# Performance work log

Hardware: AMD Instinct MI355X
Metric: run time of the kernel (lower is better)

## Reference

```python
import jax, jax.numpy as jnp
import numpy as np

D = 192          # embed_dim
DI = 2 * D       # d_inner (Mamba expand=2)
R = 12           # dt_rank = ceil(D / d_state)
N = 16           # d_state
DEPTH = 24
P = 16           # patch size
B = 4
SS, TS = 256, 128
PT = (TS // P) ** 2   # 64 template patches
PS = (SS // P) ** 2   # 256 search patches
L = PT + PS + 1       # 321 tokens (middle cls)


def setup_inputs() -> dict:
    key = jax.random.key(0)
    ks = jax.random.split(key, 24)
    f = lambda k, shp, s=0.02: (jax.random.normal(k, shp) * s).astype(jnp.float32)
    Alog = jnp.log(jnp.arange(1, N + 1, dtype=jnp.float32))  # S4D-real init
    Alog = jnp.tile(Alog, (DEPTH, DI, 1))
    return {
        "x_search": f(ks[0], (B, 3, SS, SS), 1.0),
        "x_template": f(ks[1], (B, 3, TS, TS), 1.0),
        "patch_w": f(ks[2], (D, 3, P, P)),
        "patch_b": jnp.zeros((D,), jnp.float32),
        "cls_token": f(ks[3], (1, 1, D)),
        "pos_embed": f(ks[4], (1, L, D)),
        "Win": f(ks[5], (DEPTH, 2 * DI, D)),
        "convw": f(ks[6], (DEPTH, DI, 4), 0.2),
        "convb": jnp.zeros((DEPTH, DI), jnp.float32),
        "Wx": f(ks[7], (DEPTH, R + 2 * N, DI)),
        "Wdt": f(ks[8], (DEPTH, DI, R), 0.1),
        "bdt": f(ks[9], (DEPTH, DI), 0.1),
        "Alog": Alog,
        "Dp": jnp.ones((DEPTH, DI), jnp.float32),
        "convw_b": f(ks[10], (DEPTH, DI, 4), 0.2),
        "convb_b": jnp.zeros((DEPTH, DI), jnp.float32),
        "Wx_b": f(ks[11], (DEPTH, R + 2 * N, DI)),
        "Wdt_b": f(ks[12], (DEPTH, DI, R), 0.1),
        "bdt_b": f(ks[13], (DEPTH, DI), 0.1),
        "Alog_b": Alog,
        "Dp_b": jnp.ones((DEPTH, DI), jnp.float32),
        "Wout": f(ks[14], (DEPTH, D, DI)),
        "normw": jnp.ones((DEPTH, D), jnp.float32),
        "normw_f": jnp.ones((D,), jnp.float32),
    }


def silu(x):
    return x * jax.nn.sigmoid(x)


def rmsnorm(x, w, eps=1e-5):
    return x * jax.lax.rsqrt(jnp.mean(x * x, -1, keepdims=True) + eps) * w


def patch_embed(x, w, b):
    # non-overlapping patch conv == blocked reshape + einsum
    Bn, C, H, W = x.shape
    xp = x.reshape(Bn, C, H // P, P, W // P, P)
    t = jnp.einsum('bcipjq,dcpq->bijd', xp, w)
    return t.reshape(Bn, (H // P) * (W // P), -1) + b


def causal_conv(u, w, b):
    # depthwise causal conv, kernel 4: u [B,DI,L], w [DI,4]
    Lx = u.shape[-1]
    up = jnp.pad(u, ((0, 0), (0, 0), (3, 0)))
    y = sum(w[:, k][None, :, None] * up[:, :, k:k + Lx] for k in range(4))
    return y + b[None, :, None]


def selective_scan(u, delta, A, Bm, Cm, Dp):
    # u, delta: [B,DI,L]; A: [DI,N]; Bm, Cm: [B,N,L]
    dA = jnp.exp(jnp.einsum('bdl,dn->lbdn', delta, A))
    dBu = jnp.einsum('bdl,bnl->lbdn', delta * u, Bm)

    def step(h, inp):
        dAt, dBut, ct = inp
        h = dAt * h + dBut
        return h, jnp.einsum('bdn,bn->bd', h, ct)

    h0 = jnp.zeros((u.shape[0], DI, N), u.dtype)
    _, ys = jax.lax.scan(step, h0, (dA, dBu, Cm.transpose(2, 0, 1)))
    y = ys.transpose(1, 2, 0)  # [B,DI,L]
    return y + Dp[None, :, None] * u


def _branch(x, z, convw, convb, Wx, Wdt, bdt, Alog, Dp):
    xc = silu(causal_conv(x, convw, convb))
    xdbl = jnp.einsum('bdl,ed->ble', xc, Wx)
    dt, Bm, Cm = xdbl[..., :R], xdbl[..., R:R + N], xdbl[..., R + N:]
    delta = jax.nn.softplus(jnp.einsum('blr,dr->bdl', dt, Wdt) + bdt[None, :, None])
    y = selective_scan(xc, delta, -jnp.exp(Alog), Bm.transpose(0, 2, 1),
                       Cm.transpose(0, 2, 1), Dp)
    return y * silu(z)


def _mixer(h, p):
    xz = jnp.einsum('bld,ed->ble', h, p['Win'])
    x = xz[..., :DI].transpose(0, 2, 1)   # [B,DI,L]
    z = xz[..., DI:].transpose(0, 2, 1)
    y = _branch(x, z, p['convw'], p['convb'], p['Wx'], p['Wdt'], p['bdt'],
                p['Alog'], p['Dp'])
    yb = _branch(x[..., ::-1], z[..., ::-1], p['convw_b'], p['convb_b'], p['Wx_b'],
                 p['Wdt_b'], p['bdt_b'], p['Alog_b'], p['Dp_b'])
    out = (y + yb[..., ::-1]) * 0.5  # bimamba v2 with if_divide_out
    return jnp.einsum('bdl,od->blo', out, p['Wout'])


def reference(x_search, x_template, patch_w, patch_b, cls_token, pos_embed,
              Win, convw, convb, Wx, Wdt, bdt, Alog, Dp,
              convw_b, convb_b, Wx_b, Wdt_b, bdt_b, Alog_b, Dp_b,
              Wout, normw, normw_f):
    ts = patch_embed(x_template, patch_w, patch_b)   # [B,64,D]
    ss = patch_embed(x_search, patch_w, patch_b)     # [B,256,D]
    tok = jnp.concatenate([ts, ss], 1)               # [B,320,D]
    mid = tok.shape[1] // 2
    cls = jnp.broadcast_to(cls_token, (tok.shape[0], 1, D))
    tok = jnp.concatenate([tok[:, :mid], cls, tok[:, mid:]], 1) + pos_embed

    lp = {'Win': Win, 'convw': convw, 'convb': convb, 'Wx': Wx, 'Wdt': Wdt,
          'bdt': bdt, 'Alog': Alog, 'Dp': Dp, 'convw_b': convw_b,
          'convb_b': convb_b, 'Wx_b': Wx_b, 'Wdt_b': Wdt_b, 'bdt_b': bdt_b,
          'Alog_b': Alog_b, 'Dp_b': Dp_b, 'Wout': Wout, 'normw': normw}

    def layer_step(carry, p):
        hidden, residual = carry
        residual = hidden + residual           # add
        hn = rmsnorm(residual, p['normw'])     # norm (fused_add_norm semantics)
        hidden = _mixer(hn, p)                 # mamba mixer
        return (hidden, residual), None

    (hidden, residual), _ = jax.lax.scan(layer_step, (tok, jnp.zeros_like(tok)), lp)
    return rmsnorm(hidden + residual, normw_f)   # final add + norm, [B,321,D]
```

## Files before the change

kernel.cpp:

```cpp
#include <hip/hip_runtime.h>
#include <math.h>

#define B_ 4
#define L_ 321
#define D_ 192
#define DI_ 384
#define E_ 768
#define R_ 12
#define N_ 16
#define DEPTH_ 24
#define XD 44

#define NC_ 21
#define LC_ 16

typedef __attribute__((ext_vector_type(8))) short bf16x8;
typedef __attribute__((ext_vector_type(4))) float f32x4;
typedef unsigned short ushort_t;

__device__ __forceinline__ float silu_f(float x) { return x / (1.f + __expf(-x)); }

__device__ __forceinline__ ushort_t f2bf(float x) {
    union { float f; unsigned u; } v; v.f = x;
    return (ushort_t)((v.u + 0x7fffu + ((v.u >> 16) & 1u)) >> 16);
}
__device__ __forceinline__ float bf2f(ushort_t h) {
    union { unsigned u; float f; } v; v.u = ((unsigned)h) << 16; return v.f;
}

__global__ void cvt_bf16(const float* __restrict__ src, ushort_t* __restrict__ dst, int n) {
    for (int i = blockIdx.x * blockDim.x + threadIdx.x; i < n; i += gridDim.x * blockDim.x)
        dst[i] = f2bf(src[i]);
}

__global__ void im2col_kernel(const float* __restrict__ xs, const float* __restrict__ xt,
                              ushort_t* __restrict__ pm) {
    int p_all = blockIdx.x % 320;
    int b = blockIdx.x / 320;
    const float* src; int i, j, W;
    if (p_all < 64) { int p = p_all; i = p >> 3; j = p & 7; W = 128; src = xt + (size_t)b*3*128*128; }
    else            { int p = p_all - 64; i = p >> 4; j = p & 15; W = 256; src = xs + (size_t)b*3*256*256; }
    ushort_t* dst = pm + (size_t)blockIdx.x * 768;
    for (int m = threadIdx.x; m < 768; m += blockDim.x) {
        int c = m >> 8, rem = m & 255, pp = rem >> 4, qq = rem & 15;
        dst[m] = f2bf(src[(size_t)(c*W + i*16 + pp)*W + j*16 + qq]);
    }
}

__global__ void tok_scatter(const float* __restrict__ tokmat, const float* __restrict__ pb,
                            const float* __restrict__ cls, const float* __restrict__ pos,
                            float* __restrict__ hidden, float* __restrict__ residual) {
    int blk = blockIdx.x;
    int b = blk / L_, t = blk % L_;
    int d = threadIdx.x;
    size_t o = (size_t)(b*L_ + t)*D_ + d;
    residual[o] = 0.f;
    float v;
    if (t == 160) v = cls[d];
    else {
        int p = (t < 160) ? t : t - 1;
        v = tokmat[(size_t)(b*320 + p)*D_ + d] + pb[d];
    }
    hidden[o] = v + pos[t*D_ + d];
}

template<int WM, int WN, int MFR, int NFR, int AMODE>
__device__ __forceinline__ void mfma_gemm_body(const ushort_t* __restrict__ A,
                                               const float* __restrict__ Af0,
                                               const float* __restrict__ Af1,
                                               const ushort_t* __restrict__ Bw,
                                               float* __restrict__ C,
                                               int M, int N, int K, int bx, int by) {
    constexpr int BM = WM * MFR * 16;
    constexpr int BN = WN * NFR * 16;
    int wave = threadIdx.x >> 6, lane = threadIdx.x & 63;
    int wr = wave / WN, wc = wave % WN;
    int m0 = by * BM + wr * MFR * 16;
    int n0 = bx * BN + wc * NFR * 16;
    int lrow = lane & 15;
    int lk   = (lane >> 4) * 8;

    f32x4 acc[MFR][NFR];
#pragma unroll
    for (int i = 0; i < MFR; ++i)
#pragma unroll
        for (int j = 0; j < NFR; ++j) acc[i][j] = (f32x4){0.f, 0.f, 0.f, 0.f};

    for (int k0 = 0; k0 < K; k0 += 32) {
        bf16x8 a[MFR], b[NFR];
#pragma unroll
        for (int i = 0; i < MFR; ++i) {
            int r = m0 + i*16 + lrow; r = min(r, M - 1);
            if (AMODE == 0) {
                a[i] = *(const bf16x8*)(A + (size_t)r*K + k0 + lk);
            } else {
                const float* p0 = Af0 + (size_t)r*K + k0 + lk;
                const float* p1 = Af1 + (size_t)r*K + k0 + lk;
                bf16x8 t;
#pragma unroll
                for (int j = 0; j < 8; ++j) t[j] = (short)f2bf(0.5f*(p0[j] + p1[j]));
                a[i] = t;
            }
        }
#pragma unroll
        for (int jn = 0; jn < NFR; ++jn) {
            int c = n0 + jn*16 + lrow; c = min(c, N - 1);
            b[jn] = *(const bf16x8*)(Bw + (size_t)c*K + k0 + lk);
        }
#pragma unroll
        for (int i = 0; i < MFR; ++i)
#pragma unroll
            for (int jn = 0; jn < NFR; ++jn)
                acc[i][jn] = __builtin_amdgcn_mfma_f32_16x16x32_bf16(a[i], b[jn], acc[i][jn], 0, 0, 0);
    }

    int crow = (lane >> 4) * 4;
    int ccol = lane & 15;
#pragma unroll
    for (int i = 0; i < MFR; ++i)
#pragma unroll
        for (int jn = 0; jn < NFR; ++jn) {
            int c = n0 + jn*16 + ccol;
            if (c >= N) continue;
#pragma unroll
            for (int j = 0; j < 4; ++j) {
                int r = m0 + i*16 + crow + j;
                if (r < M) C[(size_t)r*N + c] = acc[i][jn][j];
            }
        }
}

template<int WM, int WN, int MFR, int NFR, int AMODE>
__global__ __launch_bounds__(WM*WN*64) void mfma_gemm(const ushort_t* __restrict__ A,
                          const float* __restrict__ Af0, const float* __restrict__ Af1,
                          const ushort_t* __restrict__ Bw, float* __restrict__ C,
                          int M, int N, int K) {
    mfma_gemm_body<WM, WN, MFR, NFR, AMODE>(A, Af0, Af1, Bw, C, M, N, K, blockIdx.x, blockIdx.y);
}

__global__ __launch_bounds__(256) void mfma_gemm_dual(const ushort_t* __restrict__ A0, const ushort_t* __restrict__ B0, float* __restrict__ C0,
                               const ushort_t* __restrict__ A1, const ushort_t* __restrict__ B1, float* __restrict__ C1,
                               int M, int N, int K) {
    if (blockIdx.z)
        mfma_gemm_body<4, 1, 1, 3, 0>(A1, nullptr, nullptr, B1, C1, M, N, K, blockIdx.x, blockIdx.y);
    else
        mfma_gemm_body<4, 1, 1, 3, 0>(A0, nullptr, nullptr, B0, C0, M, N, K, blockIdx.x, blockIdx.y);
}

__global__ void prenorm_kernel(float* __restrict__ residual, const float* __restrict__ hidden,
                               const float* __restrict__ normw, ushort_t* __restrict__ hn) {
    int row = blockIdx.x;
    int tid = threadIdx.x;
    __shared__ float red[256];
    float v = 0.f;
    if (tid < D_) {
        v = residual[(size_t)row*D_ + tid] + hidden[(size_t)row*D_ + tid];
        residual[(size_t)row*D_ + tid] = v;
    }
    red[tid] = v * v;
    __syncthreads();
    for (int s = 128; s > 0; s >>= 1) { if (tid < s) red[tid] += red[tid + s]; __syncthreads(); }
    float scale = rsqrtf(red[0] / (float)D_ + 1e-5f);
    if (tid < D_) hn[(size_t)row*D_ + tid] = f2bf(v * scale * normw[tid]);
}

__global__ void final_kernel(const float* __restrict__ residual, const float* __restrict__ hidden,
                             const float* __restrict__ normw_f, float* __restrict__ out) {
    int row = blockIdx.x;
    int tid = threadIdx.x;
    __shared__ float red[256];
    float v = 0.f;
    if (tid < D_) v = residual[(size_t)row*D_ + tid] + hidden[(size_t)row*D_ + tid];
    red[tid] = v * v;
    __syncthreads();
    for (int s = 128; s > 0; s >>= 1) { if (tid < s) red[tid] += red[tid + s]; __syncthreads(); }
    float scale = rsqrtf(red[0] / (float)D_ + 1e-5f);
    if (tid < D_) out[(size_t)row*D_ + tid] = v * scale * normw_f[tid];
}

__global__ void conv_kernel(const ushort_t* __restrict__ xz,
                            const float* __restrict__ cw, const float* __restrict__ cb,
                            const float* __restrict__ cwb, const float* __restrict__ cbb,
                            ushort_t* __restrict__ xc_f, ushort_t* __restrict__ xc_b) {
    int blk = blockIdx.x;
    int b = blk / L_, l = blk % L_;
    int d = threadIdx.x;
    const ushort_t* xbase = xz + (size_t)b*L_*E_ + d;
    float acc = cb[d];
#pragma unroll
    for (int k = 0; k < 4; ++k) {
        int t = l - 3 + k;
        if (t >= 0) acc = fmaf(cw[d*4 + k], bf2f(xbase[(size_t)t*E_]), acc);
    }
    xc_f[(size_t)(b*L_ + l)*DI_ + d] = f2bf(silu_f(acc));
    float accb = cbb[d];
#pragma unroll
    for (int k = 0; k < 4; ++k) {
        int t = l - 3 + k;
        if (t >= 0) accb = fmaf(cwb[d*4 + k], bf2f(xbase[(size_t)(L_ - 1 - t)*E_]), accb);
    }
    xc_b[(size_t)(b*L_ + l)*DI_ + d] = f2bf(silu_f(accb));
}

__global__ void scan_part1(const ushort_t* __restrict__ xc_f, const ushort_t* __restrict__ xc_b,
                           const float* __restrict__ xdbl_f, const float* __restrict__ xdbl_b,
                           const float* __restrict__ Wdt, const float* __restrict__ bdt,
                           const float* __restrict__ Wdtb, const float* __restrict__ bdtb,
                           const float* __restrict__ Alog, const float* __restrict__ Alogb,
                           float* __restrict__ hloc, float* __restrict__ aprod) {
    int c = blockIdx.x, b = blockIdx.y, br = blockIdx.z;
    int d = threadIdx.x;
    const ushort_t* xc = br ? xc_b : xc_f;
    const float* xd = br ? xdbl_b : xdbl_f;
    const float* Wd = br ? Wdtb : Wdt;
    const float* bd = br ? bdtb : bdt;
    const float* Al = br ? Alogb : Alog;
    __shared__ float su[LC_][DI_];
    __shared__ float sdt[LC_][R_];
    __shared__ float sB[LC_][N_];
    int lbeg = c * LC_;
    int lend = min(lbeg + LC_, L_);
    int len = lend - lbeg;
    for (int l2 = 0; l2 < len; ++l2) {
        size_t row = (size_t)b*L_ + lbeg + l2;
        su[l2][d] = bf2f(xc[row*DI_ + d]);
    }
    for (int idx = d; idx < len*N_; idx += DI_) {
        int l2 = idx >> 4, n = idx & 15;
        sB[l2][n] = xd[((size_t)b*L_ + lbeg + l2)*XD + R_ + n];
    }
    for (int idx = d; idx < len*R_; idx += DI_) {
        int l2 = idx / R_, r = idx % R_;
        sdt[l2][r] = xd[((size_t)b*L_ + lbeg + l2)*XD + r];
    }
    __syncthreads();
    float wreg[R_];
#pragma unroll
    for (int r = 0; r < R_; ++r) wreg[r] = Wd[d*R_ + r];
    float bdv = bd[d];
    float a[N_];
#pragma unroll
    for (int n = 0; n < N_; ++n) a[n] = -__expf(Al[d*N_ + n]);
    float h[N_], ap[N_];
#pragma unroll
    for (int n = 0; n < N_; ++n) { h[n] = 0.f; ap[n] = 1.f; }
    for (int l2 = 0; l2 < len; ++l2) {
        float dacc = bdv;
#pragma unroll
        for (int r = 0; r < R_; ++r) dacc = fmaf(wreg[r], sdt[l2][r], dacc);
        float dv = fmaxf(dacc, 0.f) + log1pf(__expf(-fabsf(dacc)));
        float u = su[l2][d], du = dv * u;
#pragma unroll
        for (int n = 0; n < N_; ++n) {
            float e = __expf(dv * a[n]);
            h[n] = fmaf(e, h[n], du * sB[l2][n]);
            ap[n] *= e;
        }
    }
    size_t base = (((size_t)(b*2 + br)*NC_ + c)*N_)*DI_ + d;
#pragma unroll
    for (int n = 0; n < N_; ++n) {
        hloc[base + (size_t)n*DI_]  = h[n];
        aprod[base + (size_t)n*DI_] = ap[n];
    }
}

__global__ void scan_combine(const float* __restrict__ hloc, const float* __restrict__ aprod,
                             float* __restrict__ hin) {
    int g = blockIdx.x * blockDim.x + threadIdx.x;
    int bb = g / (N_ * DI_);
    int rem = g % (N_ * DI_);
    float hrun = 0.f;
    for (int c = 0; c < NC_; ++c) {
        size_t idx = ((size_t)bb*NC_ + c)*N_*DI_ + rem;
        hin[idx] = hrun;
        hrun = fmaf(aprod[idx], hrun, hloc[idx]);
    }
}

__global__ void scan_part3(const ushort_t* __restrict__ xc_f, const ushort_t* __restrict__ xc_b,
                           const float* __restrict__ xdbl_f, const float* __restrict__ xdbl_b,
                           const float* __restrict__ Wdt, const float* __restrict__ bdt,
                           const float* __restrict__ Wdtb, const float* __restrict__ bdtb,
                           const ushort_t* __restrict__ xz,
                           const float* __restrict__ Alog, const float* __restrict__ Alogb,
                           const float* __restrict__ Dpf, const float* __restrict__ Dpb,
                           const float* __restrict__ hin,
                           float* __restrict__ y_f, float* __restrict__ y_b) {
    int c = blockIdx.x, b = blockIdx.y, br = blockIdx.z;
    int d = threadIdx.x;
    const ushort_t* xc = br ? xc_b : xc_f;
    const float* xd = br ? xdbl_b : xdbl_f;
    const float* Wd = br ? Wdtb : Wdt;
    const float* bd = br ? bdtb : bdt;
    const float* Al = br ? Alogb : Alog;
    const float* Dpp = br ? Dpb : Dpf;
    float* y = br ? y_b : y_f;
    __shared__ float su[LC_][DI_];
    __shared__ float sdt[LC_][R_];
    __shared__ float sB[LC_][N_];
    __shared__ float sC[LC_][N_];
    int lbeg = c * LC_;
    int lend = min(lbeg + LC_, L_);
    int len = lend - lbeg;
    for (int l2 = 0; l2 < len; ++l2) {
        size_t row = (size_t)b*L_ + lbeg + l2;
        su[l2][d] = bf2f(xc[row*DI_ + d]);
    }
    for (int idx = d; idx < len*N_; idx += DI_) {
        int l2 = idx >> 4, n = idx & 15;
        size_t row = (size_t)b*L_ + lbeg + l2;
        sB[l2][n] = xd[row*XD + R_ + n];
        sC[l2][n] = xd[row*XD + R_ + N_ + n];
    }
    for (int idx = d; idx < len*R_; idx += DI_) {
        int l2 = idx / R_, r = idx % R_;
        sdt[l2][r] = xd[((size_t)b*L_ + lbeg + l2)*XD + r];
    }
    __syncthreads();
    float wreg[R_];
#pragma unroll
    for (int r = 0; r < R_; ++r) wreg[r] = Wd[d*R_ + r];
    float bdv = bd[d];
    float a[N_];
#pragma unroll
    for (int n = 0; n < N_; ++n) a[n] = -__expf(Al[d*N_ + n]);
    float h[N_];
    size_t hbase = (((size_t)(b*2 + br)*NC_ + c)*N_)*DI_ + d;
#pragma unroll
    for (int n = 0; n < N_; ++n) h[n] = hin[hbase + (size_t)n*DI_];
    float dpv = Dpp[d];
    for (int l2 = 0; l2 < len; ++l2) {
        float dacc = bdv;
#pragma unroll
        for (int r = 0; r < R_; ++r) dacc = fmaf(wreg[r], sdt[l2][r], dacc);
        float dv = fmaxf(dacc, 0.f) + log1pf(__expf(-fabsf(dacc)));
        float u = su[l2][d], du = dv * u;
        float yv = 0.f;
#pragma unroll
        for (int n = 0; n < N_; ++n) {
            float e = __expf(dv * a[n]);
            h[n] = fmaf(e, h[n], du * sB[l2][n]);
            yv = fmaf(h[n], sC[l2][n], yv);
        }
        yv = fmaf(dpv, u, yv);
        int lo = br ? (L_ - 1 - (lbeg + l2)) : (lbeg + l2);
        float zv = bf2f(xz[((size_t)b*L_ + lo)*E_ + DI_ + d]);
        y[((size_t)b*L_ + lo)*DI_ + d] = yv * silu_f(zv);
    }
}

extern "C" void kernel_launch(void* const* d_in, const int* in_sizes, int n_in,
                              void* d_out, int out_size, void* d_ws, size_t ws_size,
                              hipStream_t stream) {
    const float* xs     = (const float*)d_in[0];
    const float* xt     = (const float*)d_in[1];
    const float* pw     = (const float*)d_in[2];
    const float* pb     = (const float*)d_in[3];
    const float* cls    = (const float*)d_in[4];
    const float* pos    = (const float*)d_in[5];
    const float* Win    = (const float*)d_in[6];
    const float* convw  = (const float*)d_in[7];
    const float* convb  = (const float*)d_in[8];
    const float* Wx     = (const float*)d_in[9];
    const float* Wdt    = (const float*)d_in[10];
    const float* bdt    = (const float*)d_in[11];
    const float* Alog   = (const float*)d_in[12];
    const float* Dp     = (const float*)d_in[13];
    const float* convwb = (const float*)d_in[14];
    const float* convbb = (const float*)d_in[15];
    const float* Wxb    = (const float*)d_in[16];
    const float* Wdtb   = (const float*)d_in[17];
    const float* bdtb   = (const float*)d_in[18];
    const float* Alogb  = (const float*)d_in[19];
    const float* Dpb    = (const float*)d_in[20];
    const float* Wout   = (const float*)d_in[21];
    const float* normw  = (const float*)d_in[22];
    const float* normwf = (const float*)d_in[23];
    float* out = (float*)d_out;

    float* ws = (float*)d_ws;
    size_t off = 0;
    auto alloc = [&](size_t nfloats) { float* p = ws + off; off += nfloats; return p; };
    const size_t BL = (size_t)B_ * L_;
    const size_t CHNK = (size_t)B_ * 2 * NC_ * N_ * DI_;

    float*    residual = alloc(BL * D_);
    float*    hidden   = alloc(BL * D_);
    ushort_t* hn_bf    = (ushort_t*)alloc(BL * D_ / 2);
    ushort_t* xzb_bf   = (ushort_t*)alloc(BL * E_ / 2);
    ushort_t* xcf_bf   = (ushort_t*)alloc(BL * DI_ / 2);
    ushort_t* xcb_bf   = (ushort_t*)alloc(BL * DI_ / 2);
    float*    xdbl_f   = alloc(BL * XD);
    float*    xdbl_b   = alloc(BL * XD);
    float*    y_f      = alloc(BL * DI_);
    float*    y_b      = alloc(BL * DI_);
    float*    hloc     = alloc(CHNK);
    float*    aprod    = alloc(CHNK);
    float*    hin      = alloc(CHNK);
    ushort_t* pw_bf    = (ushort_t*)alloc((size_t)D_ * 768 / 2);
    ushort_t* Win_bf   = (ushort_t*)alloc((size_t)DEPTH_ * E_ * D_ / 2);
    ushort_t* Wx_bf    = (ushort_t*)alloc((size_t)DEPTH_ * XD * DI_ / 2);
    ushort_t* Wxb_bf   = (ushort_t*)alloc((size_t)DEPTH_ * XD * DI_ / 2);
    ushort_t* Wout_bf  = (ushort_t*)alloc((size_t)DEPTH_ * D_ * DI_ / 2);
    (void)ws_size; (void)in_sizes; (void)n_in; (void)out_size;

    cvt_bf16<<<dim3(64),  dim3(256), 0, stream>>>(pw,   pw_bf,   D_ * 768);
    cvt_bf16<<<dim3(2048), dim3(256), 0, stream>>>(Win,  Win_bf,  DEPTH_ * E_ * D_);
    cvt_bf16<<<dim3(512), dim3(256), 0, stream>>>(Wx,   Wx_bf,   DEPTH_ * XD * DI_);
    cvt_bf16<<<dim3(512), dim3(256), 0, stream>>>(Wxb,  Wxb_bf,  DEPTH_ * XD * DI_);
    cvt_bf16<<<dim3(1024), dim3(256), 0, stream>>>(Wout, Wout_bf, DEPTH_ * D_ * DI_);

    ushort_t* pmat   = (ushort_t*)y_f;
    float*    tokmat = y_b;
    im2col_kernel<<<dim3(B_ * 320), dim3(256), 0, stream>>>(xs, xt, pmat);
    mfma_gemm<2, 2, 2, 2, 0><<<dim3(3, 20), dim3(256), 0, stream>>>(
        pmat, nullptr, nullptr, pw_bf, tokmat, B_ * 320, D_, 768);
    tok_scatter<<<dim3(B_ * L_), dim3(192), 0, stream>>>(tokmat, pb, cls, pos, hidden, residual);

    for (int layer = 0; layer < DEPTH_; ++layer) {
        const ushort_t* Win_l  = Win_bf  + (size_t)layer * E_ * D_;
        const ushort_t* Wx_l   = Wx_bf   + (size_t)layer * XD * DI_;
        const ushort_t* Wxb_l  = Wxb_bf  + (size_t)layer * XD * DI_;
        const ushort_t* Wout_l = Wout_bf + (size_t)layer * D_ * DI_;
        const float* cw_l    = convw  + (size_t)layer * DI_ * 4;
        const float* cb_l    = convb  + (size_t)layer * DI_;
        const float* cwb_l   = convwb + (size_t)layer * DI_ * 4;
        const float* cbb_l   = convbb + (size_t)layer * DI_;
        const float* Wdt_l   = Wdt    + (size_t)layer * DI_ * R_;
        const float* Wdtb_l  = Wdtb   + (size_t)layer * DI_ * R_;
        const float* bdt_l   = bdt    + (size_t)layer * DI_;
        const float* bdtb_l  = bdtb   + (size_t)layer * DI_;
        const float* Alog_l  = Alog   + (size_t)layer * DI_ * N_;
        const float* Alogb_l = Alogb  + (size_t)layer * DI_ * N_;
        const float* Dp_l    = Dp     + (size_t)layer * DI_;
        const float* Dpb_l   = Dpb    + (size_t)layer * DI_;
        const float* normw_l = normw  + (size_t)layer * D_;

        prenorm_kernel<<<dim3((int)BL), dim3(256), 0, stream>>>(residual, hidden, normw_l, hn_bf);
        mfma_gemm<2, 2, 2, 2, 0><<<dim3(12, 21), dim3(256), 0, stream>>>(
            hn_bf, nullptr, nullptr, Win_l, hloc , (int)BL, E_, D_);
        cvt_bf16<<<dim3(1024), dim3(256), 0, stream>>>(hloc, xzb_bf, (int)(BL * E_));
        conv_kernel<<<dim3((int)BL), dim3(DI_), 0, stream>>>(xzb_bf, cw_l, cb_l, cwb_l, cbb_l, xcf_bf, xcb_bf);
        mfma_gemm_dual<<<dim3(1, 21, 2), dim3(256), 0, stream>>>(
            xcf_bf, Wx_l, xdbl_f, xcb_bf, Wxb_l, xdbl_b, (int)BL, XD, DI_);
        scan_part1<<<dim3(NC_, B_, 2), dim3(DI_), 0, stream>>>(
            xcf_bf, xcb_bf, xdbl_f, xdbl_b, Wdt_l, bdt_l, Wdtb_l, bdtb_l,
            Alog_l, Alogb_l, hloc, aprod);
        scan_combine<<<dim3((B_*2*N_*DI_)/256), dim3(256), 0, stream>>>(hloc, aprod, hin);
        scan_part3<<<dim3(NC_, B_, 2), dim3(DI_), 0, stream>>>(
            xcf_bf, xcb_bf, xdbl_f, xdbl_b, Wdt_l, bdt_l, Wdtb_l, bdtb_l, xzb_bf,
            Alog_l, Alogb_l, Dp_l, Dpb_l, hin, y_f, y_b);
        mfma_gemm<2, 2, 2, 2, 1><<<dim3(3, 21), dim3(256), 0, stream>>>(
            nullptr, y_f, y_b, Wout_l, hidden, (int)BL, D_, DI_);
    }

    final_kernel<<<dim3((int)BL), dim3(256), 0, stream>>>(residual, hidden, normwf, out);
}
```

Before: 2.152 ms.

## Fuse conv into x-proj GEMM, out-proj with add+norm, bf16 in-proj output

The in-projection GEMM now writes bf16 directly, which drops the separate fp32-to-bf16 conversion pass. The causal depthwise conv plus SiLU is computed inside the x-projection MFMA kernel. The output projection is fused with the residual add and RMSNorm of the next layer, or the final norm on the last layer, which removes the per-layer prenorm and final kernels. Scan inner loops get a partial unroll for full-length chunks. Together these cut launches and memory round trips, at the cost of redundant conv reads per row tile and lower occupancy in the fused out-proj with only 41 blocks.

```diff
diff --git a/kernel.cpp b/kernel.cpp
--- a/kernel.cpp
+++ b/kernel.cpp
@@ -64,15 +64,14 @@
     hidden[o] = v + pos[t*D_ + d];
 }
 
-template<int WM, int WN, int MFR, int NFR, int AMODE>
-__device__ __forceinline__ void mfma_gemm_body(const ushort_t* __restrict__ A,
-                                               const float* __restrict__ Af0,
-                                               const float* __restrict__ Af1,
-                                               const ushort_t* __restrict__ Bw,
-                                               float* __restrict__ C,
-                                               int M, int N, int K, int bx, int by) {
+template<int WM, int WN, int MFR, int NFR, int CMODE>
+__global__ __launch_bounds__(WM*WN*64) void mfma_gemm(const ushort_t* __restrict__ A,
+                          const ushort_t* __restrict__ Bw,
+                          float* __restrict__ Cf, ushort_t* __restrict__ Ch,
+                          int M, int N, int K) {
     constexpr int BM = WM * MFR * 16;
     constexpr int BN = WN * NFR * 16;
+    int bx = blockIdx.x, by = blockIdx.y;
     int wave = threadIdx.x >> 6, lane = threadIdx.x & 63;
     int wr = wave / WN, wc = wave % WN;
     int m0 = by * BM + wr * MFR * 16;
@@ -91,16 +90,7 @@
 #pragma unroll
         for (int i = 0; i < MFR; ++i) {
             int r = m0 + i*16 + lrow; r = min(r, M - 1);
-            if (AMODE == 0) {
-                a[i] = *(const bf16x8*)(A + (size_t)r*K + k0 + lk);
-            } else {
-                const float* p0 = Af0 + (size_t)r*K + k0 + lk;
-                const float* p1 = Af1 + (size_t)r*K + k0 + lk;
-                bf16x8 t;
-#pragma unroll
-                for (int j = 0; j < 8; ++j) t[j] = (short)f2bf(0.5f*(p0[j] + p1[j]));
-                a[i] = t;
-            }
+            a[i] = *(const bf16x8*)(A + (size_t)r*K + k0 + lk);
         }
 #pragma unroll
         for (int jn = 0; jn < NFR; ++jn) {
@@ -125,26 +115,175 @@
 #pragma unroll
             for (int j = 0; j < 4; ++j) {
                 int r = m0 + i*16 + crow + j;
-                if (r < M) C[(size_t)r*N + c] = acc[i][jn][j];
+                if (r < M) {
+                    if (CMODE == 0) Cf[(size_t)r*N + c] = acc[i][jn][j];
+                    else            Ch[(size_t)r*N + c] = f2bf(acc[i][jn][j]);
+                }
             }
         }
 }
 
-template<int WM, int WN, int MFR, int NFR, int AMODE>
-__global__ __launch_bounds__(WM*WN*64) void mfma_gemm(const ushort_t* __restrict__ A,
-                          const float* __restrict__ Af0, const float* __restrict__ Af1,
-                          const ushort_t* __restrict__ Bw, float* __restrict__ C,
-                          int M, int N, int K) {
-    mfma_gemm_body<WM, WN, MFR, NFR, AMODE>(A, Af0, Af1, Bw, C, M, N, K, blockIdx.x, blockIdx.y);
-}
-
-__global__ __launch_bounds__(256) void mfma_gemm_dual(const ushort_t* __restrict__ A0, const ushort_t* __restrict__ B0, float* __restrict__ C0,
-                               const ushort_t* __restrict__ A1, const ushort_t* __restrict__ B1, float* __restrict__ C1,
-                               int M, int N, int K) {
-    if (blockIdx.z)
-        mfma_gemm_body<4, 1, 1, 3, 0>(A1, nullptr, nullptr, B1, C1, M, N, K, blockIdx.x, blockIdx.y);
-    else
-        mfma_gemm_body<4, 1, 1, 3, 0>(A0, nullptr, nullptr, B0, C0, M, N, K, blockIdx.x, blockIdx.y);
+__global__ __launch_bounds__(256) void conv_xdbl_dual(
+    const ushort_t* __restrict__ xz,
+    const float* __restrict__ cw, const float* __restrict__ cb,
+    const float* __restrict__ cwb, const float* __restrict__ cbb,
+    const ushort_t* __restrict__ Wxf, const ushort_t* __restrict__ Wxbw,
+    ushort_t* __restrict__ xc_f, ushort_t* __restrict__ xc_b,
+    float* __restrict__ xdbl_f, float* __restrict__ xdbl_b) {
+    constexpr int NFR = 3;
+    const int M = B_ * L_, Nn = XD, K = DI_;
+    int rev = blockIdx.z;
+    const float* cwp = rev ? cwb : cw;
+    const float* cbp = rev ? cbb : cb;
+    const ushort_t* Bw = rev ? Wxbw : Wxf;
+    ushort_t* xc = rev ? xc_b : xc_f;
+    float* Cout = rev ? xdbl_b : xdbl_f;
+
+    int wave = threadIdx.x >> 6, lane = threadIdx.x & 63;
+    int m0 = blockIdx.y * 64 + wave * 16;
+    int lrow = lane & 15;
+    int lk = (lane >> 4) * 8;
+
+    f32x4 acc[NFR];
+#pragma unroll
+    for (int jn = 0; jn < NFR; ++jn) acc[jn] = (f32x4){0.f, 0.f, 0.f, 0.f};
+
+    int rc = min(m0 + lrow, M - 1);
+    int b = rc / L_, l = rc % L_;
+    const ushort_t* xzb = xz + (size_t)b*L_*E_;
+
+    for (int k0 = 0; k0 < K; k0 += 32) {
+        int d0 = k0 + lk;
+        float xr[4][8];
+#pragma unroll
+        for (int k = 0; k < 4; ++k) {
+            int t = l - 3 + k;
+            if (t >= 0) {
+                int tr = rev ? (L_ - 1 - t) : t;
+                bf16x8 xv = *(const bf16x8*)(xzb + (size_t)tr*E_ + d0);
+#pragma unroll
+                for (int j = 0; j < 8; ++j) xr[k][j] = bf2f((ushort_t)xv[j]);
+            } else {
+#pragma unroll
+                for (int j = 0; j < 8; ++j) xr[k][j] = 0.f;
+            }
+        }
+        bf16x8 afrag;
+#pragma unroll
+        for (int j = 0; j < 8; ++j) {
+            float4 w4 = *(const float4*)(cwp + (size_t)(d0 + j) * 4);
+            float acv = cbp[d0 + j];
+            acv = fmaf(w4.x, xr[0][j], acv);
+            acv = fmaf(w4.y, xr[1][j], acv);
+            acv = fmaf(w4.z, xr[2][j], acv);
+            acv = fmaf(w4.w, xr[3][j], acv);
+            afrag[j] = (short)f2bf(silu_f(acv));
+        }
+        *(bf16x8*)(xc + (size_t)rc*DI_ + d0) = afrag;
+        bf16x8 bfr[NFR];
+#pragma unroll
+        for (int jn = 0; jn < NFR; ++jn) {
+            int c = min(jn*16 + lrow, Nn - 1);
+            bfr[jn] = *(const bf16x8*)(Bw + (size_t)c*K + k0 + lk);
+        }
+#pragma unroll
+        for (int jn = 0; jn < NFR; ++jn)
+            acc[jn] = __builtin_amdgcn_mfma_f32_16x16x32_bf16(afrag, bfr[jn], acc[jn], 0, 0, 0);
+    }
+    int crow = (lane >> 4) * 4, ccol = lane & 15;
+#pragma unroll
+    for (int jn = 0; jn < NFR; ++jn) {
+        int c = jn*16 + ccol;
+        if (c >= Nn) continue;
+#pragma unroll
+        for (int j = 0; j < 4; ++j) {
+            int rr = m0 + crow + j;
+            if (rr < M) Cout[(size_t)rr*Nn + c] = acc[jn][j];
+        }
+    }
+}
+
+template<bool LAST>
+__global__ __launch_bounds__(512) void outproj_fused(
+    const float* __restrict__ yf, const float* __restrict__ yb,
+    const ushort_t* __restrict__ Ww,
+    float* __restrict__ residual, const float* __restrict__ nw,
+    ushort_t* __restrict__ hn, float* __restrict__ outp) {
+    const int M = B_*L_, Nn = D_, K = DI_;
+    int wave = threadIdx.x >> 6, lane = threadIdx.x & 63;
+    int wr = wave >> 2, wc = wave & 3;
+    int m0 = blockIdx.x * 32 + wr * 16;
+    int n0 = wc * 48;
+    int lrow = lane & 15, lk = (lane >> 4) * 8;
+
+    f32x4 acc[3];
+#pragma unroll
+    for (int jn = 0; jn < 3; ++jn) acc[jn] = (f32x4){0.f, 0.f, 0.f, 0.f};
+
+    for (int k0 = 0; k0 < K; k0 += 32) {
+        int r = min(m0 + lrow, M - 1);
+        const float* p0 = yf + (size_t)r*K + k0 + lk;
+        const float* p1 = yb + (size_t)r*K + k0 + lk;
+        bf16x8 a;
+#pragma unroll
+        for (int j = 0; j < 8; ++j) a[j] = (short)f2bf(0.5f*(p0[j] + p1[j]));
+        bf16x8 bfr[3];
+#pragma unroll
+        for (int jn = 0; jn < 3; ++jn) {
+            int c = n0 + jn*16 + lrow;
+            bfr[jn] = *(const bf16x8*)(Ww + (size_t)c*K + k0 + lk);
+        }
+#pragma unroll
+        for (int jn = 0; jn < 3; ++jn)
+            acc[jn] = __builtin_amdgcn_mfma_f32_16x16x32_bf16(a, bfr[jn], acc[jn], 0, 0, 0);
+    }
+
+    int crow = (lane >> 4) * 4, ccol = lane & 15;
+    float resv[4][3];
+    float sq[4] = {0.f, 0.f, 0.f, 0.f};
+#pragma unroll
+    for (int j = 0; j < 4; ++j) {
+        int r = m0 + crow + j;
+        bool ok = r < M;
+#pragma unroll
+        for (int jn = 0; jn < 3; ++jn) {
+            int c = n0 + jn*16 + ccol;
+            float v = ok ? (residual[(size_t)r*Nn + c] + acc[jn][j]) : 0.f;
+            resv[j][jn] = v;
+            sq[j] = fmaf(v, v, sq[j]);
+        }
+    }
+#pragma unroll
+    for (int m = 1; m < 16; m <<= 1)
+#pragma unroll
+        for (int j = 0; j < 4; ++j) sq[j] += __shfl_xor(sq[j], m, 64);
+
+    __shared__ float part[32][4];
+    if (ccol == 0) {
+        int rt0 = wr*16 + crow;
+#pragma unroll
+        for (int j = 0; j < 4; ++j) part[rt0 + j][wc] = sq[j];
+    }
+    __syncthreads();
+#pragma unroll
+    for (int j = 0; j < 4; ++j) {
+        int r = m0 + crow + j;
+        if (r >= M) continue;
+        int rt = wr*16 + crow + j;
+        float tot = part[rt][0] + part[rt][1] + part[rt][2] + part[rt][3];
+        float scale = rsqrtf(tot / (float)Nn + 1e-5f);
+#pragma unroll
+        for (int jn = 0; jn < 3; ++jn) {
+            int c = n0 + jn*16 + ccol;
+            float v = resv[j][jn];
+            if (LAST) {
+                outp[(size_t)r*Nn + c] = v * scale * nw[c];
+            } else {
+                residual[(size_t)r*Nn + c] = v;
+                hn[(size_t)r*Nn + c] = f2bf(v * scale * nw[c]);
+            }
+        }
+    }
 }
 
 __global__ void prenorm_kernel(float* __restrict__ residual, const float* __restrict__ hidden,
@@ -162,44 +301,6 @@
     for (int s = 128; s > 0; s >>= 1) { if (tid < s) red[tid] += red[tid + s]; __syncthreads(); }
     float scale = rsqrtf(red[0] / (float)D_ + 1e-5f);
     if (tid < D_) hn[(size_t)row*D_ + tid] = f2bf(v * scale * normw[tid]);
-}
-
-__global__ void final_kernel(const float* __restrict__ residual, const float* __restrict__ hidden,
-                             const float* __restrict__ normw_f, float* __restrict__ out) {
-    int row = blockIdx.x;
-    int tid = threadIdx.x;
-    __shared__ float red[256];
-    float v = 0.f;
-    if (tid < D_) v = residual[(size_t)row*D_ + tid] + hidden[(size_t)row*D_ + tid];
-    red[tid] = v * v;
-    __syncthreads();
-    for (int s = 128; s > 0; s >>= 1) { if (tid < s) red[tid] += red[tid + s]; __syncthreads(); }
-    float scale = rsqrtf(red[0] / (float)D_ + 1e-5f);
-    if (tid < D_) out[(size_t)row*D_ + tid] = v * scale * normw_f[tid];
-}
-
-__global__ void conv_kernel(const ushort_t* __restrict__ xz,
-                            const float* __restrict__ cw, const float* __restrict__ cb,
-                            const float* __restrict__ cwb, const float* __restrict__ cbb,
-                            ushort_t* __restrict__ xc_f, ushort_t* __restrict__ xc_b) {
-    int blk = blockIdx.x;
-    int b = blk / L_, l = blk % L_;
-    int d = threadIdx.x;
-    const ushort_t* xbase = xz + (size_t)b*L_*E_ + d;
-    float acc = cb[d];
-#pragma unroll
-    for (int k = 0; k < 4; ++k) {
-        int t = l - 3 + k;
-        if (t >= 0) acc = fmaf(cw[d*4 + k], bf2f(xbase[(size_t)t*E_]), acc);
-    }
-    xc_f[(size_t)(b*L_ + l)*DI_ + d] = f2bf(silu_f(acc));
-    float accb = cbb[d];
-#pragma unroll
-    for (int k = 0; k < 4; ++k) {
-        int t = l - 3 + k;
-        if (t >= 0) accb = fmaf(cwb[d*4 + k], bf2f(xbase[(size_t)(L_ - 1 - t)*E_]), accb);
-    }
-    xc_b[(size_t)(b*L_ + l)*DI_ + d] = f2bf(silu_f(accb));
 }
 
 __global__ void scan_part1(const ushort_t* __restrict__ xc_f, const ushort_t* __restrict__ xc_b,
@@ -244,7 +345,8 @@
     float h[N_], ap[N_];
 #pragma unroll
     for (int n = 0; n < N_; ++n) { h[n] = 0.f; ap[n] = 1.f; }
-    for (int l2 = 0; l2 < len; ++l2) {
+
+    auto step = [&](int l2) {
         float dacc = bdv;
 #pragma unroll
         for (int r = 0; r < R_; ++r) dacc = fmaf(wreg[r], sdt[l2][r], dacc);
@@ -256,6 +358,12 @@
             h[n] = fmaf(e, h[n], du * sB[l2][n]);
             ap[n] *= e;
         }
+    };
+    if (len == LC_) {
+#pragma unroll 4
+        for (int l2 = 0; l2 < LC_; ++l2) step(l2);
+    } else {
+        for (int l2 = 0; l2 < len; ++l2) step(l2);
     }
     size_t base = (((size_t)(b*2 + br)*NC_ + c)*N_)*DI_ + d;
 #pragma unroll
@@ -330,7 +438,8 @@
 #pragma unroll
     for (int n = 0; n < N_; ++n) h[n] = hin[hbase + (size_t)n*DI_];
     float dpv = Dpp[d];
-    for (int l2 = 0; l2 < len; ++l2) {
+
+    auto step = [&](int l2) {
         float dacc = bdv;
 #pragma unroll
         for (int r = 0; r < R_; ++r) dacc = fmaf(wreg[r], sdt[l2][r], dacc);
@@ -347,6 +456,12 @@
         int lo = br ? (L_ - 1 - (lbeg + l2)) : (lbeg + l2);
         float zv = bf2f(xz[((size_t)b*L_ + lo)*E_ + DI_ + d]);
         y[((size_t)b*L_ + lo)*DI_ + d] = yv * silu_f(zv);
+    };
+    if (len == LC_) {
+#pragma unroll 4
+        for (int l2 = 0; l2 < LC_; ++l2) step(l2);
+    } else {
+        for (int l2 = 0; l2 < len; ++l2) step(l2);
     }
 }
 
@@ -405,18 +520,19 @@
     ushort_t* Wout_bf  = (ushort_t*)alloc((size_t)DEPTH_ * D_ * DI_ / 2);
     (void)ws_size; (void)in_sizes; (void)n_in; (void)out_size;
 
-    cvt_bf16<<<dim3(64),  dim3(256), 0, stream>>>(pw,   pw_bf,   D_ * 768);
+    cvt_bf16<<<dim3(64),   dim3(256), 0, stream>>>(pw,   pw_bf,   D_ * 768);
     cvt_bf16<<<dim3(2048), dim3(256), 0, stream>>>(Win,  Win_bf,  DEPTH_ * E_ * D_);
-    cvt_bf16<<<dim3(512), dim3(256), 0, stream>>>(Wx,   Wx_bf,   DEPTH_ * XD * DI_);
-    cvt_bf16<<<dim3(512), dim3(256), 0, stream>>>(Wxb,  Wxb_bf,  DEPTH_ * XD * DI_);
+    cvt_bf16<<<dim3(512),  dim3(256), 0, stream>>>(Wx,   Wx_bf,   DEPTH_ * XD * DI_);
+    cvt_bf16<<<dim3(512),  dim3(256), 0, stream>>>(Wxb,  Wxb_bf,  DEPTH_ * XD * DI_);
     cvt_bf16<<<dim3(1024), dim3(256), 0, stream>>>(Wout, Wout_bf, DEPTH_ * D_ * DI_);
 
     ushort_t* pmat   = (ushort_t*)y_f;
     float*    tokmat = y_b;
     im2col_kernel<<<dim3(B_ * 320), dim3(256), 0, stream>>>(xs, xt, pmat);
     mfma_gemm<2, 2, 2, 2, 0><<<dim3(3, 20), dim3(256), 0, stream>>>(
-        pmat, nullptr, nullptr, pw_bf, tokmat, B_ * 320, D_, 768);
+        pmat, pw_bf, tokmat, nullptr, B_ * 320, D_, 768);
     tok_scatter<<<dim3(B_ * L_), dim3(192), 0, stream>>>(tokmat, pb, cls, pos, hidden, residual);
+    prenorm_kernel<<<dim3((int)BL), dim3(256), 0, stream>>>(residual, hidden, normw, hn_bf);
 
     for (int layer = 0; layer < DEPTH_; ++layer) {
         const ushort_t* Win_l  = Win_bf  + (size_t)layer * E_ * D_;
@@ -435,15 +551,12 @@
         const float* Alogb_l = Alogb  + (size_t)layer * DI_ * N_;
         const float* Dp_l    = Dp     + (size_t)layer * DI_;
         const float* Dpb_l   = Dpb    + (size_t)layer * DI_;
-        const float* normw_l = normw  + (size_t)layer * D_;
-
-        prenorm_kernel<<<dim3((int)BL), dim3(256), 0, stream>>>(residual, hidden, normw_l, hn_bf);
-        mfma_gemm<2, 2, 2, 2, 0><<<dim3(12, 21), dim3(256), 0, stream>>>(
-            hn_bf, nullptr, nullptr, Win_l, hloc , (int)BL, E_, D_);
-        cvt_bf16<<<dim3(1024), dim3(256), 0, stream>>>(hloc, xzb_bf, (int)(BL * E_));
-        conv_kernel<<<dim3((int)BL), dim3(DI_), 0, stream>>>(xzb_bf, cw_l, cb_l, cwb_l, cbb_l, xcf_bf, xcb_bf);
-        mfma_gemm_dual<<<dim3(1, 21, 2), dim3(256), 0, stream>>>(
-            xcf_bf, Wx_l, xdbl_f, xcb_bf, Wxb_l, xdbl_b, (int)BL, XD, DI_);
+
+        mfma_gemm<2, 2, 2, 2, 1><<<dim3(12, 21), dim3(256), 0, stream>>>(
+            hn_bf, Win_l, nullptr, xzb_bf, (int)BL, E_, D_);
+        conv_xdbl_dual<<<dim3(1, 21, 2), dim3(256), 0, stream>>>(
+            xzb_bf, cw_l, cb_l, cwb_l, cbb_l, Wx_l, Wxb_l,
+            xcf_bf, xcb_bf, xdbl_f, xdbl_b);
         scan_part1<<<dim3(NC_, B_, 2), dim3(DI_), 0, stream>>>(
             xcf_bf, xcb_bf, xdbl_f, xdbl_b, Wdt_l, bdt_l, Wdtb_l, bdtb_l,
             Alog_l, Alogb_l, hloc, aprod);
@@ -451,9 +564,12 @@
         scan_part3<<<dim3(NC_, B_, 2), dim3(DI_), 0, stream>>>(
             xcf_bf, xcb_bf, xdbl_f, xdbl_b, Wdt_l, bdt_l, Wdtb_l, bdtb_l, xzb_bf,
             Alog_l, Alogb_l, Dp_l, Dpb_l, hin, y_f, y_b);
-        mfma_gemm<2, 2, 2, 2, 1><<<dim3(3, 21), dim3(256), 0, stream>>>(
-            nullptr, y_f, y_b, Wout_l, hidden, (int)BL, D_, DI_);
-    }
-
-    final_kernel<<<dim3((int)BL), dim3(256), 0, stream>>>(residual, hidden, normwf, out);
-}
+        if (layer < DEPTH_ - 1) {
+            outproj_fused<false><<<dim3(41), dim3(512), 0, stream>>>(
+                y_f, y_b, Wout_l, residual, normw + (size_t)(layer + 1) * D_, hn_bf, nullptr);
+        } else {
+            outproj_fused<true><<<dim3(41), dim3(512), 0, stream>>>(
+                y_f, y_b, Wout_l, residual, normwf, nullptr, out);
+        }
+    }
+}
```

Result: slower. 2.586 ms (+20.2%).

## Fuse bf16 epilogue into in-proj GEMM, split scans, add small-tile GEMMs

Applied to the files above, without the earlier changes.

The in-projection GEMM now writes bf16 directly, which removes the separate fp32 store and conversion pass per layer. The x_dbl and out-projection GEMMs move to dedicated single-wave kernels with small tiles, giving more blocks on a small M. The scan kernels split DI across two 192-thread blocks to double the grid, and unroll the full-chunk loop. In exchange, the in-proj output is rounded once more and each block does less work, so per-block overhead rises.

```diff
diff --git a/kernel.cpp b/kernel.cpp
--- a/kernel.cpp
+++ b/kernel.cpp
@@ -64,15 +64,14 @@
     hidden[o] = v + pos[t*D_ + d];
 }
 
-template<int WM, int WN, int MFR, int NFR, int AMODE>
-__device__ __forceinline__ void mfma_gemm_body(const ushort_t* __restrict__ A,
-                                               const float* __restrict__ Af0,
-                                               const float* __restrict__ Af1,
-                                               const ushort_t* __restrict__ Bw,
-                                               float* __restrict__ C,
-                                               int M, int N, int K, int bx, int by) {
+template<int WM, int WN, int MFR, int NFR, int CMODE>
+__global__ __launch_bounds__(WM*WN*64) void mfma_gemm(const ushort_t* __restrict__ A,
+                          const ushort_t* __restrict__ Bw,
+                          float* __restrict__ Cf, ushort_t* __restrict__ Ch,
+                          int M, int N, int K) {
     constexpr int BM = WM * MFR * 16;
     constexpr int BN = WN * NFR * 16;
+    int bx = blockIdx.x, by = blockIdx.y;
     int wave = threadIdx.x >> 6, lane = threadIdx.x & 63;
     int wr = wave / WN, wc = wave % WN;
     int m0 = by * BM + wr * MFR * 16;
@@ -91,16 +90,7 @@
 #pragma unroll
         for (int i = 0; i < MFR; ++i) {
             int r = m0 + i*16 + lrow; r = min(r, M - 1);
-            if (AMODE == 0) {
-                a[i] = *(const bf16x8*)(A + (size_t)r*K + k0 + lk);
-            } else {
-                const float* p0 = Af0 + (size_t)r*K + k0 + lk;
-                const float* p1 = Af1 + (size_t)r*K + k0 + lk;
-                bf16x8 t;
-#pragma unroll
-                for (int j = 0; j < 8; ++j) t[j] = (short)f2bf(0.5f*(p0[j] + p1[j]));
-                a[i] = t;
-            }
+            a[i] = *(const bf16x8*)(A + (size_t)r*K + k0 + lk);
         }
 #pragma unroll
         for (int jn = 0; jn < NFR; ++jn) {
@@ -125,26 +115,108 @@
 #pragma unroll
             for (int j = 0; j < 4; ++j) {
                 int r = m0 + i*16 + crow + j;
-                if (r < M) C[(size_t)r*N + c] = acc[i][jn][j];
+                if (r < M) {
+                    if (CMODE == 0) Cf[(size_t)r*N + c] = acc[i][jn][j];
+                    else            Ch[(size_t)r*N + c] = f2bf(acc[i][jn][j]);
+                }
             }
         }
 }
 
-template<int WM, int WN, int MFR, int NFR, int AMODE>
-__global__ __launch_bounds__(WM*WN*64) void mfma_gemm(const ushort_t* __restrict__ A,
-                          const float* __restrict__ Af0, const float* __restrict__ Af1,
-                          const ushort_t* __restrict__ Bw, float* __restrict__ C,
-                          int M, int N, int K) {
-    mfma_gemm_body<WM, WN, MFR, NFR, AMODE>(A, Af0, Af1, Bw, C, M, N, K, blockIdx.x, blockIdx.y);
-}
-
-__global__ __launch_bounds__(256) void mfma_gemm_dual(const ushort_t* __restrict__ A0, const ushort_t* __restrict__ B0, float* __restrict__ C0,
-                               const ushort_t* __restrict__ A1, const ushort_t* __restrict__ B1, float* __restrict__ C1,
-                               int M, int N, int K) {
-    if (blockIdx.z)
-        mfma_gemm_body<4, 1, 1, 3, 0>(A1, nullptr, nullptr, B1, C1, M, N, K, blockIdx.x, blockIdx.y);
-    else
-        mfma_gemm_body<4, 1, 1, 3, 0>(A0, nullptr, nullptr, B0, C0, M, N, K, blockIdx.x, blockIdx.y);
+__global__ __launch_bounds__(64) void xdbl_dual(
+    const ushort_t* __restrict__ xcf, const ushort_t* __restrict__ xcb,
+    const ushort_t* __restrict__ Wxf, const ushort_t* __restrict__ Wxbw,
+    float* __restrict__ xdf, float* __restrict__ xdb) {
+    const int M = B_ * L_;
+    int rev = blockIdx.y;
+    const ushort_t* A  = rev ? xcb : xcf;
+    const ushort_t* Bw = rev ? Wxbw : Wxf;
+    float* C = rev ? xdb : xdf;
+    int lane = threadIdx.x;
+    int m0 = blockIdx.x * 16;
+    int lrow = lane & 15, lk = (lane >> 4) * 8;
+
+    f32x4 acc[3];
+#pragma unroll
+    for (int jn = 0; jn < 3; ++jn) acc[jn] = (f32x4){0.f, 0.f, 0.f, 0.f};
+
+    for (int k0 = 0; k0 < DI_; k0 += 32) {
+        int r = min(m0 + lrow, M - 1);
+        bf16x8 a = *(const bf16x8*)(A + (size_t)r*DI_ + k0 + lk);
+        bf16x8 b[3];
+#pragma unroll
+        for (int jn = 0; jn < 3; ++jn) {
+            int c = min(jn*16 + lrow, XD - 1);
+            b[jn] = *(const bf16x8*)(Bw + (size_t)c*DI_ + k0 + lk);
+        }
+#pragma unroll
+        for (int jn = 0; jn < 3; ++jn)
+            acc[jn] = __builtin_amdgcn_mfma_f32_16x16x32_bf16(a, b[jn], acc[jn], 0, 0, 0);
+    }
+    int crow = (lane >> 4) * 4, ccol = lane & 15;
+#pragma unroll
+    for (int jn = 0; jn < 3; ++jn) {
+        int c = jn*16 + ccol;
+        if (c >= XD) continue;
+#pragma unroll
+        for (int j = 0; j < 4; ++j) {
+            int r = m0 + crow + j;
+            if (r < M) C[(size_t)r*XD + c] = acc[jn][j];
+        }
+    }
+}
+
+__global__ __launch_bounds__(64) void outproj_gemm(
+    const float* __restrict__ yf, const float* __restrict__ yb,
+    const ushort_t* __restrict__ Ww, float* __restrict__ hidden) {
+    const int M = B_*L_, Nn = D_, K = DI_;
+    int lane = threadIdx.x;
+    int m0 = blockIdx.y * 32;
+    int n0 = blockIdx.x * 48;
+    int lrow = lane & 15, lk = (lane >> 4) * 8;
+
+    f32x4 acc[2][3];
+#pragma unroll
+    for (int i = 0; i < 2; ++i)
+#pragma unroll
+        for (int jn = 0; jn < 3; ++jn) acc[i][jn] = (f32x4){0.f, 0.f, 0.f, 0.f};
+
+    for (int k0 = 0; k0 < K; k0 += 32) {
+        bf16x8 a[2];
+#pragma unroll
+        for (int i = 0; i < 2; ++i) {
+            int r = min(m0 + i*16 + lrow, M - 1);
+            const float* p0 = yf + (size_t)r*K + k0 + lk;
+            const float* p1 = yb + (size_t)r*K + k0 + lk;
+            bf16x8 t;
+#pragma unroll
+            for (int j = 0; j < 8; ++j) t[j] = (short)f2bf(0.5f*(p0[j] + p1[j]));
+            a[i] = t;
+        }
+        bf16x8 b[3];
+#pragma unroll
+        for (int jn = 0; jn < 3; ++jn) {
+            int c = n0 + jn*16 + lrow;
+            b[jn] = *(const bf16x8*)(Ww + (size_t)c*K + k0 + lk);
+        }
+#pragma unroll
+        for (int i = 0; i < 2; ++i)
+#pragma unroll
+            for (int jn = 0; jn < 3; ++jn)
+                acc[i][jn] = __builtin_amdgcn_mfma_f32_16x16x32_bf16(a[i], b[jn], acc[i][jn], 0, 0, 0);
+    }
+    int crow = (lane >> 4) * 4, ccol = lane & 15;
+#pragma unroll
+    for (int i = 0; i < 2; ++i)
+#pragma unroll
+        for (int jn = 0; jn < 3; ++jn) {
+            int c = n0 + jn*16 + ccol;
+#pragma unroll
+            for (int j = 0; j < 4; ++j) {
+                int r = m0 + i*16 + crow + j;
+                if (r < M) hidden[(size_t)r*Nn + c] = acc[i][jn][j];
+            }
+        }
 }
 
 __global__ void prenorm_kernel(float* __restrict__ residual, const float* __restrict__ hidden,
@@ -202,20 +274,22 @@
     xc_b[(size_t)(b*L_ + l)*DI_ + d] = f2bf(silu_f(accb));
 }
 
-__global__ void scan_part1(const ushort_t* __restrict__ xc_f, const ushort_t* __restrict__ xc_b,
+__global__ __launch_bounds__(192) void scan_part1(
+                           const ushort_t* __restrict__ xc_f, const ushort_t* __restrict__ xc_b,
                            const float* __restrict__ xdbl_f, const float* __restrict__ xdbl_b,
                            const float* __restrict__ Wdt, const float* __restrict__ bdt,
                            const float* __restrict__ Wdtb, const float* __restrict__ bdtb,
                            const float* __restrict__ Alog, const float* __restrict__ Alogb,
                            float* __restrict__ hloc, float* __restrict__ aprod) {
-    int c = blockIdx.x, b = blockIdx.y, br = blockIdx.z;
-    int d = threadIdx.x;
+    int c = blockIdx.x, b = blockIdx.y >> 1, half = blockIdx.y & 1, br = blockIdx.z;
+    int tid = threadIdx.x;
+    int d = half * 192 + tid;
     const ushort_t* xc = br ? xc_b : xc_f;
     const float* xd = br ? xdbl_b : xdbl_f;
     const float* Wd = br ? Wdtb : Wdt;
     const float* bd = br ? bdtb : bdt;
     const float* Al = br ? Alogb : Alog;
-    __shared__ float su[LC_][DI_];
+    __shared__ float su[LC_][192];
     __shared__ float sdt[LC_][R_];
     __shared__ float sB[LC_][N_];
     int lbeg = c * LC_;
@@ -223,13 +297,13 @@
     int len = lend - lbeg;
     for (int l2 = 0; l2 < len; ++l2) {
         size_t row = (size_t)b*L_ + lbeg + l2;
-        su[l2][d] = bf2f(xc[row*DI_ + d]);
-    }
-    for (int idx = d; idx < len*N_; idx += DI_) {
+        su[l2][tid] = bf2f(xc[row*DI_ + d]);
+    }
+    for (int idx = tid; idx < len*N_; idx += 192) {
         int l2 = idx >> 4, n = idx & 15;
         sB[l2][n] = xd[((size_t)b*L_ + lbeg + l2)*XD + R_ + n];
     }
-    for (int idx = d; idx < len*R_; idx += DI_) {
+    for (int idx = tid; idx < len*R_; idx += 192) {
         int l2 = idx / R_, r = idx % R_;
         sdt[l2][r] = xd[((size_t)b*L_ + lbeg + l2)*XD + r];
     }
@@ -244,18 +318,25 @@
     float h[N_], ap[N_];
 #pragma unroll
     for (int n = 0; n < N_; ++n) { h[n] = 0.f; ap[n] = 1.f; }
-    for (int l2 = 0; l2 < len; ++l2) {
+
+    auto step = [&](int l2) {
         float dacc = bdv;
 #pragma unroll
         for (int r = 0; r < R_; ++r) dacc = fmaf(wreg[r], sdt[l2][r], dacc);
         float dv = fmaxf(dacc, 0.f) + log1pf(__expf(-fabsf(dacc)));
-        float u = su[l2][d], du = dv * u;
+        float u = su[l2][tid], du = dv * u;
 #pragma unroll
         for (int n = 0; n < N_; ++n) {
             float e = __expf(dv * a[n]);
             h[n] = fmaf(e, h[n], du * sB[l2][n]);
             ap[n] *= e;
         }
+    };
+    if (len == LC_) {
+#pragma unroll 4
+        for (int l2 = 0; l2 < LC_; ++l2) step(l2);
+    } else {
+        for (int l2 = 0; l2 < len; ++l2) step(l2);
     }
     size_t base = (((size_t)(b*2 + br)*NC_ + c)*N_)*DI_ + d;
 #pragma unroll
@@ -278,7 +359,8 @@
     }
 }
 
-__global__ void scan_part3(const ushort_t* __restrict__ xc_f, const ushort_t* __restrict__ xc_b,
+__global__ __launch_bounds__(192) void scan_part3(
+                           const ushort_t* __restrict__ xc_f, const ushort_t* __restrict__ xc_b,
                            const float* __restrict__ xdbl_f, const float* __restrict__ xdbl_b,
                            const float* __restrict__ Wdt, const float* __restrict__ bdt,
                            const float* __restrict__ Wdtb, const float* __restrict__ bdtb,
@@ -287,8 +369,9 @@
                            const float* __restrict__ Dpf, const float* __restrict__ Dpb,
                            const float* __restrict__ hin,
                            float* __restrict__ y_f, float* __restrict__ y_b) {
-    int c = blockIdx.x, b = blockIdx.y, br = blockIdx.z;
-    int d = threadIdx.x;
+    int c = blockIdx.x, b = blockIdx.y >> 1, half = blockIdx.y & 1, br = blockIdx.z;
+    int tid = threadIdx.x;
+    int d = half * 192 + tid;
     const ushort_t* xc = br ? xc_b : xc_f;
     const float* xd = br ? xdbl_b : xdbl_f;
     const float* Wd = br ? Wdtb : Wdt;
@@ -296,7 +379,7 @@
     const float* Al = br ? Alogb : Alog;
     const float* Dpp = br ? Dpb : Dpf;
     float* y = br ? y_b : y_f;
-    __shared__ float su[LC_][DI_];
+    __shared__ float su[LC_][192];
     __shared__ float sdt[LC_][R_];
     __shared__ float sB[LC_][N_];
     __shared__ float sC[LC_][N_];
@@ -305,15 +388,15 @@
     int len = lend - lbeg;
     for (int l2 = 0; l2 < len; ++l2) {
         size_t row = (size_t)b*L_ + lbeg + l2;
-        su[l2][d] = bf2f(xc[row*DI_ + d]);
-    }
-    for (int idx = d; idx < len*N_; idx += DI_) {
+        su[l2][tid] = bf2f(xc[row*DI_ + d]);
+    }
+    for (int idx = tid; idx < len*N_; idx += 192) {
         int l2 = idx >> 4, n = idx & 15;
         size_t row = (size_t)b*L_ + lbeg + l2;
         sB[l2][n] = xd[row*XD + R_ + n];
         sC[l2][n] = xd[row*XD + R_ + N_ + n];
     }
-    for (int idx = d; idx < len*R_; idx += DI_) {
+    for (int idx = tid; idx < len*R_; idx += 192) {
         int l2 = idx / R_, r = idx % R_;
         sdt[l2][r] = xd[((size_t)b*L_ + lbeg + l2)*XD + r];
     }
@@ -330,12 +413,13 @@
 #pragma unroll
     for (int n = 0; n < N_; ++n) h[n] = hin[hbase + (size_t)n*DI_];
     float dpv = Dpp[d];
-    for (int l2 = 0; l2 < len; ++l2) {
+
+    auto step = [&](int l2) {
         float dacc = bdv;
 #pragma unroll
         for (int r = 0; r < R_; ++r) dacc = fmaf(wreg[r], sdt[l2][r], dacc);
         float dv = fmaxf(dacc, 0.f) + log1pf(__expf(-fabsf(dacc)));
-        float u = su[l2][d], du = dv * u;
+        float u = su[l2][tid], du = dv * u;
         float yv = 0.f;
 #pragma unroll
         for (int n = 0; n < N_; ++n) {
@@ -347,6 +431,12 @@
         int lo = br ? (L_ - 1 - (lbeg + l2)) : (lbeg + l2);
         float zv = bf2f(xz[((size_t)b*L_ + lo)*E_ + DI_ + d]);
         y[((size_t)b*L_ + lo)*DI_ + d] = yv * silu_f(zv);
+    };
+    if (len == LC_) {
+#pragma unroll 4
+        for (int l2 = 0; l2 < LC_; ++l2) step(l2);
+    } else {
+        for (int l2 = 0; l2 < len; ++l2) step(l2);
     }
 }
 
@@ -405,17 +495,17 @@
     ushort_t* Wout_bf  = (ushort_t*)alloc((size_t)DEPTH_ * D_ * DI_ / 2);
     (void)ws_size; (void)in_sizes; (void)n_in; (void)out_size;
 
-    cvt_bf16<<<dim3(64),  dim3(256), 0, stream>>>(pw,   pw_bf,   D_ * 768);
+    cvt_bf16<<<dim3(64),   dim3(256), 0, stream>>>(pw,   pw_bf,   D_ * 768);
     cvt_bf16<<<dim3(2048), dim3(256), 0, stream>>>(Win,  Win_bf,  DEPTH_ * E_ * D_);
-    cvt_bf16<<<dim3(512), dim3(256), 0, stream>>>(Wx,   Wx_bf,   DEPTH_ * XD * DI_);
-    cvt_bf16<<<dim3(512), dim3(256), 0, stream>>>(Wxb,  Wxb_bf,  DEPTH_ * XD * DI_);
+    cvt_bf16<<<dim3(512),  dim3(256), 0, stream>>>(Wx,   Wx_bf,   DEPTH_ * XD * DI_);
+    cvt_bf16<<<dim3(512),  dim3(256), 0, stream>>>(Wxb,  Wxb_bf,  DEPTH_ * XD * DI_);
     cvt_bf16<<<dim3(1024), dim3(256), 0, stream>>>(Wout, Wout_bf, DEPTH_ * D_ * DI_);
 
     ushort_t* pmat   = (ushort_t*)y_f;
     float*    tokmat = y_b;
     im2col_kernel<<<dim3(B_ * 320), dim3(256), 0, stream>>>(xs, xt, pmat);
     mfma_gemm<2, 2, 2, 2, 0><<<dim3(3, 20), dim3(256), 0, stream>>>(
-        pmat, nullptr, nullptr, pw_bf, tokmat, B_ * 320, D_, 768);
+        pmat, pw_bf, tokmat, nullptr, B_ * 320, D_, 768);
     tok_scatter<<<dim3(B_ * L_), dim3(192), 0, stream>>>(tokmat, pb, cls, pos, hidden, residual);
 
     for (int layer = 0; layer < DEPTH_; ++layer) {
@@ -438,21 +528,20 @@
         const float* normw_l = normw  + (size_t)layer * D_;
 
         prenorm_kernel<<<dim3((int)BL), dim3(256), 0, stream>>>(residual, hidden, normw_l, hn_bf);
-        mfma_gemm<2, 2, 2, 2, 0><<<dim3(12, 21), dim3(256), 0, stream>>>(
-            hn_bf, nullptr, nullptr, Win_l, hloc , (int)BL, E_, D_);
-        cvt_bf16<<<dim3(1024), dim3(256), 0, stream>>>(hloc, xzb_bf, (int)(BL * E_));
-        conv_kernel<<<dim3((int)BL), dim3(DI_), 0, stream>>>(xzb_bf, cw_l, cb_l, cwb_l, cbb_l, xcf_bf, xcb_bf);
-        mfma_gemm_dual<<<dim3(1, 21, 2), dim3(256), 0, stream>>>(
-            xcf_bf, Wx_l, xdbl_f, xcb_bf, Wxb_l, xdbl_b, (int)BL, XD, DI_);
-        scan_part1<<<dim3(NC_, B_, 2), dim3(DI_), 0, stream>>>(
+        mfma_gemm<2, 2, 2, 2, 1><<<dim3(12, 21), dim3(256), 0, stream>>>(
+            hn_bf, Win_l, nullptr, xzb_bf, (int)BL, E_, D_);
+        conv_kernel<<<dim3((int)BL), dim3(DI_), 0, stream>>>(
+            xzb_bf, cw_l, cb_l, cwb_l, cbb_l, xcf_bf, xcb_bf);
+        xdbl_dual<<<dim3(81, 2), dim3(64), 0, stream>>>(
+            xcf_bf, xcb_bf, Wx_l, Wxb_l, xdbl_f, xdbl_b);
+        scan_part1<<<dim3(NC_, B_ * 2, 2), dim3(192), 0, stream>>>(
             xcf_bf, xcb_bf, xdbl_f, xdbl_b, Wdt_l, bdt_l, Wdtb_l, bdtb_l,
             Alog_l, Alogb_l, hloc, aprod);
         scan_combine<<<dim3((B_*2*N_*DI_)/256), dim3(256), 0, stream>>>(hloc, aprod, hin);
-        scan_part3<<<dim3(NC_, B_, 2), dim3(DI_), 0, stream>>>(
+        scan_part3<<<dim3(NC_, B_ * 2, 2), dim3(192), 0, stream>>>(
             xcf_bf, xcb_bf, xdbl_f, xdbl_b, Wdt_l, bdt_l, Wdtb_l, bdtb_l, xzb_bf,
             Alog_l, Alogb_l, Dp_l, Dpb_l, hin, y_f, y_b);
-        mfma_gemm<2, 2, 2, 2, 1><<<dim3(3, 21), dim3(256), 0, stream>>>(
-            nullptr, y_f, y_b, Wout_l, hidden, (int)BL, D_, DI_);
+        outproj_gemm<<<dim3(4, 41), dim3(64), 0, stream>>>(y_f, y_b, Wout_l, hidden);
     }
 
     final_kernel<<<dim3((int)BL), dim3(256), 0, stream>>>(residual, hidden, normwf, out);
```

New measurement: 1.941 ms. 1.11x faster.
